# Kernel tuning notes

Hardware: AMD Instinct MI355X
Metric: run time of the kernel (lower is better)

## Reference

```python
import jax, jax.numpy as jnp
import numpy as np

B, S, H, NH = 2, 2048, 1024, 16
DK = H // NH

def setup_inputs() -> dict:
    key = jax.random.key(0)
    ks = jax.random.split(key, 12)
    scale = 0.02
    return {
        "Q": jax.random.normal(ks[0], (B, S, H), jnp.float32),
        "K": jax.random.normal(ks[1], (B, S, H), jnp.float32),
        "V": jax.random.normal(ks[2], (B, S, H), jnp.float32),
        "attn_mask": jax.random.randint(ks[3], (B, S, S), 0, 2).astype(bool),
        "Wq": jax.random.normal(ks[4], (H, H), jnp.float32) * scale,
        "bq": jnp.zeros((H,), jnp.float32),
        "Wk": jax.random.normal(ks[5], (H, H), jnp.float32) * scale,
        "bk": jnp.zeros((H,), jnp.float32),
        "Wv": jax.random.normal(ks[6], (H, H), jnp.float32) * scale,
        "bv": jnp.zeros((H,), jnp.float32),
        "Wo": jax.random.normal(ks[7], (H, H), jnp.float32) * scale,
        "bo": jnp.zeros((H,), jnp.float32),
    }

def reference(Q, K, V, attn_mask, Wq, bq, Wk, bk, Wv, bv, Wo, bo):
    b = Q.shape[0]
    # linear projections (torch nn.Linear: x @ W.T + b), split heads -> [b, nh, s, dk]
    def proj(x, W, bias):
        return (x @ W.T + bias).reshape(b, -1, NH, DK).transpose(0, 2, 1, 3)
    q = proj(Q, Wq, bq)
    k = proj(K, Wk, bk)
    v = proj(V, Wv, bv)
    scores = jnp.einsum("bhqd,bhkd->bhqk", q, k) / jnp.sqrt(jnp.float32(DK))
    scores = jnp.where(attn_mask[:, None, :, :], jnp.float32(-1e9), scores)
    attn = jax.nn.softmax(scores, axis=-1)  # dropout prob = 0.0 (identity)
    ctx = jnp.einsum("bhqk,bhkd->bhqd", attn, v)
    ctx = ctx.transpose(0, 2, 1, 3).reshape(b, -1, NH * DK)
    return ctx @ Wo.T + bo
```

## Files before the change

kernel.cpp:

```cpp
#include <hip/hip_runtime.h>

typedef short s16x8 __attribute__((ext_vector_type(8)));
typedef float f32x4 __attribute__((ext_vector_type(4)));
typedef unsigned short u16;
typedef unsigned int u32;
typedef unsigned long long u64;

#define DEVI __device__ __forceinline__

#if __has_builtin(__builtin_amdgcn_exp2f)
#define EXP2F(x) __builtin_amdgcn_exp2f(x)
#else
#define EXP2F(x) exp2f(x)
#endif

#define QSCALE 0.1803368801111204f

DEVI float bf2f(u16 u){ union { u32 i; float f; } v; v.i = ((u32)u) << 16; return v.f; }
DEVI u16 f2bf(float f){ union { float f; u32 i; } v; v.f = f; u32 u = v.i;
                        return (u16)((u + 0x7fffu + ((u >> 16) & 1u)) >> 16); }
DEVI u32 pack2r(float a, float b){
  union { float f; u32 i; } ua, ub; ua.f = a; ub.f = b;
  return ((ua.i + 0x8000u) >> 16) | ((ub.i + 0x8000u) & 0xffff0000u);
}
DEVI u64 pack4(float a, float b, float c, float d){
  return (u64)f2bf(a) | ((u64)f2bf(b) << 16) | ((u64)f2bf(c) << 32) | ((u64)f2bf(d) << 48);
}

DEVI f32x4 mfma_bf16(s16x8 a, s16x8 b, f32x4 c){
  return __builtin_amdgcn_mfma_f32_16x16x32_bf16(a, b, c, 0, 0, 0);
}

#define GLDS(gp, lp) __builtin_amdgcn_global_load_lds( \
    (const __attribute__((address_space(1))) void*)(gp), \
    (__attribute__((address_space(3))) void*)(lp), 16, 0, 0)

DEVI float4 cvt8f32(const float* p){
  float4 x = *(const float4*)p;
  float4 y = *(const float4*)(p + 4);
  union { u16 t[8]; float4 f4; } u;
  u.t[0] = f2bf(x.x); u.t[1] = f2bf(x.y); u.t[2] = f2bf(x.z); u.t[3] = f2bf(x.w);
  u.t[4] = f2bf(y.x); u.t[5] = f2bf(y.y); u.t[6] = f2bf(y.z); u.t[7] = f2bf(y.w);
  return u.f4;
}

DEVI bool detect_f32(const u16* probe){
  __shared__ int dsum[4];
  const int tid = threadIdx.x;
  int bad = 0;
#pragma unroll
  for (int i = 0; i < 16; ++i){
    u16 u = probe[tid * 16 + i];
    int e = (u >> 7) & 0xFF;
    bad += (e != 0 && (e < 100 || e > 150)) ? 1 : 0;
  }
#pragma unroll
  for (int o = 1; o < 64; o <<= 1) bad += __shfl_xor(bad, o);
  if ((tid & 63) == 0) dsum[tid >> 6] = bad;
  __syncthreads();
  bool r = (dsum[0] + dsum[1] + dsum[2] + dsum[3]) > 64;
  __syncthreads();
  return r;
}

struct PrepArgs { const void* src[7]; void* dst[7]; u32 coff[8]; };

__global__ __launch_bounds__(256) void prep(PrepArgs a, const u16* probe){
  const bool f32 = detect_f32(probe);
  if (!f32) return;
  const u32 total = a.coff[7];
  for (u32 c = blockIdx.x * 256 + threadIdx.x; c < total; c += gridDim.x * 256){
    int s = 0;
#pragma unroll
    for (int i = 1; i < 7; ++i) s += (c >= a.coff[i]) ? 1 : 0;
    u32 lc = c - a.coff[s];
    ((float4*)a.dst[s])[lc] = cvt8f32((const float*)a.src[s] + (size_t)lc * 8);
  }
}

__global__ __launch_bounds__(256) void maskpack(const int* __restrict__ mask,
                                                u64* __restrict__ bits){
  const int lane = threadIdx.x & 63, wid = threadIdx.x >> 6;
  const int row = blockIdx.x * 4 + wid;
  const int* mrow = mask + (size_t)row * 2048;
  for (int c = 0; c < 32; ++c){
    int v = mrow[c * 64 + lane];
    u64 w = __ballot(v == 0);
    if (lane == 0) bits[(size_t)row * 32 + c] = w;
  }
}

struct ProjP {
  const void* X[3];   const u16* Xc[3];
  const void* W[3];   const u16* Wc[3];
  const void* bias[3];
  u16* out[3];
  const u16* probe;
  int conv_ok;
};

__global__ __launch_bounds__(256) void proj_gemm(ProjP p){
  __shared__ u16 As[128 * 64];
  __shared__ u16 Bs[128 * 64];
  const int z = blockIdx.z;
  const bool in32 = detect_f32(p.probe);
  const bool f32st = in32 && !p.conv_ok;
  const u16* Ab = (in32 && p.conv_ok) ? p.Xc[z] : (const u16*)p.X[z];
  const u16* Wb = (in32 && p.conv_ok) ? p.Wc[z] : (const u16*)p.W[z];
  const float* Af = (const float*)p.X[z];
  const float* Wf = (const float*)p.W[z];
  const int tid = threadIdx.x;
  const int lane = tid & 63, wid = tid >> 6;
  const int quad = lane >> 4, l15 = lane & 15;
  const int m0 = blockIdx.y * 128, n0 = blockIdx.x * 128;
  const int wm = (wid >> 1) * 64, wn = (wid & 1) * 64;
  const int K = 1024;

  f32x4 acc[4][4];
  const f32x4 z4 = {0.f, 0.f, 0.f, 0.f};
  for (int i = 0; i < 4; ++i) for (int j = 0; j < 4; ++j) acc[i][j] = z4;

  for (int ko = 0; ko < 16; ++ko){
    const int kk = ko * 64;
    if (f32st){
#pragma unroll
      for (int i = 0; i < 4; ++i){
        int g = tid * 4 + i;
        int row = g >> 3, c = g & 7;
        *(float4*)(As + row * 64 + ((c ^ (row & 7)) * 8)) =
            cvt8f32(Af + (size_t)(m0 + row) * K + kk + c * 8);
        *(float4*)(Bs + row * 64 + ((c ^ (row & 7)) * 8)) =
            cvt8f32(Wf + (size_t)(n0 + row) * K + kk + c * 8);
      }
    } else {
#pragma unroll
      for (int i = 0; i < 4; ++i){
        int ci = (wid * 4 + i) * 64 + lane;
        int row = ci >> 3, gcc = (ci & 7) ^ (row & 7);
        GLDS(Ab + (size_t)(m0 + row) * K + kk + gcc * 8, As + (size_t)(wid * 4 + i) * 512);
        GLDS(Wb + (size_t)(n0 + row) * K + kk + gcc * 8, Bs + (size_t)(wid * 4 + i) * 512);
      }
    }
    __syncthreads();
#pragma unroll
    for (int ks = 0; ks < 2; ++ks){
      s16x8 af[4], bfr[4];
#pragma unroll
      for (int mt = 0; mt < 4; ++mt){
        int row = wm + mt * 16 + l15;
        af[mt] = *(const s16x8*)(As + row * 64 + (((ks * 4 + quad) ^ (row & 7)) * 8));
      }
#pragma unroll
      for (int nt = 0; nt < 4; ++nt){
        int row = wn + nt * 16 + l15;
        bfr[nt] = *(const s16x8*)(Bs + row * 64 + (((ks * 4 + quad) ^ (row & 7)) * 8));
      }
#pragma unroll
      for (int mt = 0; mt < 4; ++mt)
#pragma unroll
        for (int nt = 0; nt < 4; ++nt)
          acc[mt][nt] = mfma_bf16(af[mt], bfr[nt], acc[mt][nt]);
    }
    __syncthreads();
  }

  u16* outp = p.out[z];
#pragma unroll
  for (int nt = 0; nt < 4; ++nt){
    int col = n0 + wn + nt * 16 + l15;
    float bv = in32 ? ((const float*)p.bias[z])[col] : bf2f(((const u16*)p.bias[z])[col]);
#pragma unroll
    for (int mt = 0; mt < 4; ++mt){
      if (z == 2){
        int srow = m0 + wm + mt * 16 + quad * 4;
        int b = srow >> 11, s = srow & 2047, hh = col >> 6, d = col & 63;
        size_t idx = (((size_t)(b * 16 + hh)) * 64 + d) * 2048 + s;
        *(u64*)(outp + idx) = pack4(acc[mt][nt][0] + bv, acc[mt][nt][1] + bv,
                                    acc[mt][nt][2] + bv, acc[mt][nt][3] + bv);
      } else {
#pragma unroll
        for (int r = 0; r < 4; ++r){
          int row = m0 + wm + mt * 16 + quad * 4 + r;
          float v = acc[mt][nt][r] + bv;
          if (z == 0) v *= QSCALE;
          int b = row >> 11, s = row & 2047, hh = col >> 6, d = col & 63;
          outp[(((size_t)(b * 16 + hh)) * 2048 + s) * 64 + d] = f2bf(v);
        }
      }
    }
  }
}

__global__ __launch_bounds__(256) void gemm_out(const u16* __restrict__ A,
                                                const void* __restrict__ Wv,
                                                const u16* __restrict__ Wbf,
                                                const void* __restrict__ biasv,
                                                void* __restrict__ outv,
                                                const u16* __restrict__ probe,
                                                int conv_ok){
  __shared__ u16 As[64 * 64];
  __shared__ u16 Bs[128 * 64];
  const bool in32 = detect_f32(probe);
  const bool f32st = in32 && !conv_ok;
  const u16* Wb = (in32 && conv_ok) ? Wbf : (const u16*)Wv;
  const float* Wf = (const float*)Wv;
  const int tid = threadIdx.x;
  const int lane = tid & 63, wid = tid >> 6;
  const int quad = lane >> 4, l15 = lane & 15;
  const int m0 = blockIdx.y * 64, n0 = blockIdx.x * 128;
  const int wm = (wid >> 1) * 32, wn = (wid & 1) * 64;
  const int K = 1024;

  f32x4 acc[2][4];
  const f32x4 z4 = {0.f, 0.f, 0.f, 0.f};
  for (int i = 0; i < 2; ++i) for (int j = 0; j < 4; ++j) acc[i][j] = z4;

  for (int ko = 0; ko < 16; ++ko){
    const int kk = ko * 64;
#pragma unroll
    for (int i = 0; i < 2; ++i){
      int ci = (wid * 2 + i) * 64 + lane;
      int row = ci >> 3, gcc = (ci & 7) ^ (row & 7);
      GLDS(A + (size_t)(m0 + row) * K + kk + gcc * 8, As + (size_t)(wid * 2 + i) * 512);
    }
    if (f32st){
#pragma unroll
      for (int i = 0; i < 4; ++i){
        int g = tid * 4 + i;
        int row = g >> 3, c = g & 7;
        *(float4*)(Bs + row * 64 + ((c ^ (row & 7)) * 8)) =
            cvt8f32(Wf + (size_t)(n0 + row) * K + kk + c * 8);
      }
    } else {
#pragma unroll
      for (int i = 0; i < 4; ++i){
        int ci = (wid * 4 + i) * 64 + lane;
        int row = ci >> 3, gcc = (ci & 7) ^ (row & 7);
        GLDS(Wb + (size_t)(n0 + row) * K + kk + gcc * 8, Bs + (size_t)(wid * 4 + i) * 512);
      }
    }
    __syncthreads();
#pragma unroll
    for (int ks = 0; ks < 2; ++ks){
      s16x8 af[2], bfr[4];
#pragma unroll
      for (int mt = 0; mt < 2; ++mt){
        int row = wm + mt * 16 + l15;
        af[mt] = *(const s16x8*)(As + row * 64 + (((ks * 4 + quad) ^ (row & 7)) * 8));
      }
#pragma unroll
      for (int nt = 0; nt < 4; ++nt){
        int row = wn + nt * 16 + l15;
        bfr[nt] = *(const s16x8*)(Bs + row * 64 + (((ks * 4 + quad) ^ (row & 7)) * 8));
      }
#pragma unroll
      for (int mt = 0; mt < 2; ++mt)
#pragma unroll
        for (int nt = 0; nt < 4; ++nt)
          acc[mt][nt] = mfma_bf16(af[mt], bfr[nt], acc[mt][nt]);
    }
    __syncthreads();
  }

#pragma unroll
  for (int nt = 0; nt < 4; ++nt){
    int col = n0 + wn + nt * 16 + l15;
    float bv = in32 ? ((const float*)biasv)[col] : bf2f(((const u16*)biasv)[col]);
#pragma unroll
    for (int mt = 0; mt < 2; ++mt)
#pragma unroll
      for (int r = 0; r < 4; ++r){
        int row = m0 + wm + mt * 16 + quad * 4 + r;
        float v = acc[mt][nt][r] + bv;
        size_t idx = (size_t)row * 1024 + col;
        if (in32) ((float*)outv)[idx] = v;
        else      ((u16*)outv)[idx]   = f2bf(v);
      }
  }
}

__global__ __launch_bounds__(256) void attn2(const u16* __restrict__ qws,
                                             const u16* __restrict__ kws,
                                             const u16* __restrict__ vtws,
                                             const u64* __restrict__ mbits,
                                             const int* __restrict__ rawmask,
                                             int use_raw,
                                             u16* __restrict__ ctxws){
  __shared__ u16 Ks[64 * 64];
  __shared__ u16 Vt[64 * 64];
  __shared__ u16 Ps[4][16 * 64];
  const int tid = threadIdx.x;
  const int lane = tid & 63, wid = tid >> 6;
  const int quad = lane >> 4, l15 = lane & 15;
  const int h = blockIdx.x, qt = blockIdx.y, b = blockIdx.z;
  const int q0 = qt * 64;
  const size_t bh = (size_t)(b * 16 + h) * (2048 * 64);
  const int qrow = q0 + wid * 16 + l15;

  s16x8 qf[2];
#pragma unroll
  for (int ks = 0; ks < 2; ++ks)
    qf[ks] = *(const s16x8*)(qws + bh + (size_t)qrow * 64 + ks * 32 + quad * 8);

  const f32x4 z4 = {0.f, 0.f, 0.f, 0.f};
  f32x4 ctx[4];
  for (int dt = 0; dt < 4; ++dt) ctx[dt] = z4;
  float lr = 0.f;

  u16* pp = &Ps[wid][0];
  u32 pw[4];
#pragma unroll
  for (int ntk = 0; ntk < 4; ++ntk)
    pw[ntk] = l15 * 64 + (((u32)(ntk * 2 + (quad >> 1)) ^ (u32)(l15 & 7)) * 8) + (quad & 1) * 4;

  const u64* mrow = mbits + ((size_t)(b * 2048 + qrow)) * 32;

  for (int kt = 0; kt < 32; ++kt){
    const int k0 = kt * 64;
#pragma unroll
    for (int i = 0; i < 2; ++i){
      int ci = (wid * 2 + i) * 64 + lane;
      int row = ci >> 3, gcc = (ci & 7) ^ (row & 7);
      GLDS(kws + bh + (size_t)(k0 + row) * 64 + gcc * 8, Ks + (size_t)(wid * 2 + i) * 512);
      GLDS(vtws + bh + (size_t)row * 2048 + k0 + gcc * 8, Vt + (size_t)(wid * 2 + i) * 512);
    }
    __syncthreads();

    f32x4 s[4];
    for (int ntk = 0; ntk < 4; ++ntk) s[ntk] = z4;
#pragma unroll
    for (int ks = 0; ks < 2; ++ks)
#pragma unroll
      for (int ntk = 0; ntk < 4; ++ntk){
        int row = ntk * 16 + l15;
        s16x8 kf = *(const s16x8*)(Ks + row * 64 + (((ks * 4 + quad) ^ (row & 7)) * 8));
        s[ntk] = mfma_bf16(kf, qf[ks], s[ntk]);
      }

    float ls = 0.f;
    if (!use_raw){
      u64 w = mrow[kt] >> (quad * 4);
      u32 wlo = (u32)w, whi = (u32)(w >> 32);
#pragma unroll
      for (int ntk = 0; ntk < 4; ++ntk){
        u32 half = (ntk < 2) ? wlo : whi;
#pragma unroll
        for (int r = 0; r < 4; ++r){
          float pv = EXP2F(s[ntk][r]);
          u32 bit = (half >> ((ntk & 1) * 16 + r)) & 1u;
          pv *= (float)bit;
          s[ntk][r] = pv;
          ls += pv;
        }
      }
    } else {
#pragma unroll
      for (int ntk = 0; ntk < 4; ++ntk)
#pragma unroll
        for (int r = 0; r < 4; ++r){
          int key = k0 + ntk * 16 + quad * 4 + r;
          int mv = rawmask[((size_t)(b * 2048 + qrow)) * 2048 + key];
          float pv = EXP2F(s[ntk][r]);
          pv = mv ? 0.f : pv;
          s[ntk][r] = pv;
          ls += pv;
        }
    }
    lr += ls;

#pragma unroll
    for (int ntk = 0; ntk < 4; ++ntk){
      uint2 t;
      t.x = pack2r(s[ntk][0], s[ntk][1]);
      t.y = pack2r(s[ntk][2], s[ntk][3]);
      *(uint2*)(pp + pw[ntk]) = t;
    }
    s16x8 pf[2];
#pragma unroll
    for (int ks = 0; ks < 2; ++ks)
      pf[ks] = *(const s16x8*)(pp + l15 * 64 + (((ks * 4 + quad) ^ (l15 & 7)) * 8));

#pragma unroll
    for (int ks = 0; ks < 2; ++ks)
#pragma unroll
      for (int dt = 0; dt < 4; ++dt){
        int row = dt * 16 + l15;
        s16x8 vf = *(const s16x8*)(Vt + row * 64 + (((ks * 4 + quad) ^ (row & 7)) * 8));
        ctx[dt] = mfma_bf16(vf, pf[ks], ctx[dt]);
      }
    __syncthreads();
  }

  lr += __shfl_xor(lr, 16);
  lr += __shfl_xor(lr, 32);
  float inv = 1.0f / fmaxf(lr, 1e-30f);

#pragma unroll
  for (int dt = 0; dt < 4; ++dt){
    int d0 = dt * 16 + quad * 4;
    u64 w = pack4(ctx[dt][0] * inv, ctx[dt][1] * inv, ctx[dt][2] * inv, ctx[dt][3] * inv);
    *(u64*)(ctxws + ((size_t)(b * 2048 + qrow)) * 1024 + h * 64 + d0) = w;
  }
}

extern "C" void kernel_launch(void* const* d_in, const int* in_sizes, int n_in,
                              void* d_out, int out_size, void* d_ws, size_t ws_size,
                              hipStream_t stream){
  const void* Q    = d_in[0];
  const void* Kin  = d_in[1];
  const void* Vin  = d_in[2];
  const int* mask  = (const int*)d_in[3];
  const void* Wq = d_in[4];  const void* bq = d_in[5];
  const void* Wk = d_in[6];  const void* bk = d_in[7];
  const void* Wv = d_in[8];  const void* bv = d_in[9];
  const void* Wo = d_in[10]; const void* bo = d_in[11];

  char* ws = (char*)d_ws;
  const size_t MB = 1u << 20;
  const bool small_ws = ws_size < 33 * MB;
  const bool big_ws   = ws_size >= 66 * MB;
  u64* mbits = (u64*)ws;
  const size_t base = small_ws ? 0 : MB;
  u16* qws  = (u16*)(ws + base);
  u16* kws  = (u16*)(ws + base + 8 * MB);
  u16* vtws = (u16*)(ws + base + 16 * MB);
  u16* cws  = (u16*)(ws + base + 24 * MB);
  u16* Qc  = (u16*)(ws + 33 * MB);
  u16* Kc  = (u16*)(ws + 41 * MB);
  u16* Vc  = (u16*)(ws + 49 * MB);
  u16* Wqc = (u16*)(ws + 57 * MB);
  u16* Wkc = (u16*)(ws + 59 * MB);
  u16* Wvc = (u16*)(ws + 61 * MB);
  u16* Woc = (u16*)(ws + 63 * MB);
  const u16* probe = (const u16*)Q;

  if (big_ws){
    PrepArgs pa;
    pa.src[0] = Q;  pa.src[1] = Kin; pa.src[2] = Vin;
    pa.src[3] = Wq; pa.src[4] = Wk;  pa.src[5] = Wv; pa.src[6] = Wo;
    pa.dst[0] = Qc;  pa.dst[1] = Kc;  pa.dst[2] = Vc;
    pa.dst[3] = Wqc; pa.dst[4] = Wkc; pa.dst[5] = Wvc; pa.dst[6] = Woc;
    const u32 cq = 4194304 / 8, cw = 1048576 / 8;
    pa.coff[0] = 0;
    pa.coff[1] = cq;          pa.coff[2] = 2 * cq;      pa.coff[3] = 3 * cq;
    pa.coff[4] = 3 * cq + cw; pa.coff[5] = 3 * cq + 2 * cw;
    pa.coff[6] = 3 * cq + 3 * cw; pa.coff[7] = 3 * cq + 4 * cw;
    prep<<<dim3(2048), 256, 0, stream>>>(pa, probe);
  }

  if (!small_ws)
    maskpack<<<dim3(1024), 256, 0, stream>>>(mask, mbits);

  ProjP pp;
  pp.X[0] = Q;  pp.X[1] = Kin; pp.X[2] = Vin;
  pp.Xc[0] = Qc; pp.Xc[1] = Kc; pp.Xc[2] = Vc;
  pp.W[0] = Wq; pp.W[1] = Wk; pp.W[2] = Wv;
  pp.Wc[0] = Wqc; pp.Wc[1] = Wkc; pp.Wc[2] = Wvc;
  pp.bias[0] = bq; pp.bias[1] = bk; pp.bias[2] = bv;
  pp.out[0] = qws; pp.out[1] = kws; pp.out[2] = vtws;
  pp.probe = probe;
  pp.conv_ok = big_ws ? 1 : 0;
  proj_gemm<<<dim3(8, 32, 3), 256, 0, stream>>>(pp);

  attn2<<<dim3(16, 32, 2), 256, 0, stream>>>(qws, kws, vtws, mbits, mask,
                                             small_ws ? 1 : 0, cws);

  gemm_out<<<dim3(8, 64), 256, 0, stream>>>(cws, Wo, Woc, bo, d_out, probe,
                                            big_ws ? 1 : 0);
}
```

Before: 292.6 us.

## Split attention over key range, compute row sums via MFMA, mask via bitwise AND

Splits the key loop of the attention kernel into two halves across extra blocks (split-K), writing partial normalized contexts and row sums, then adds a combine kernel that merges them. The row sum of probabilities is now accumulated with an extra MFMA against a ones vector instead of scalar adds and shuffles. Mask application becomes a bitwise AND on packed bf16 pairs. These are meant to raise occupancy and parallelism (grid of 1024 blocks is doubled) and cut VALU work, at the cost of extra partial-result traffic, an extra launch, and a bf16 rounding of the partials before combining.

```diff
diff --git a/kernel.cpp b/kernel.cpp
--- a/kernel.cpp
+++ b/kernel.cpp
@@ -25,6 +25,9 @@
 }
 DEVI u64 pack4(float a, float b, float c, float d){
   return (u64)f2bf(a) | ((u64)f2bf(b) << 16) | ((u64)f2bf(c) << 32) | ((u64)f2bf(d) << 48);
+}
+DEVI u32 expand2(u32 t){
+  return ((t & 1u) * 0xFFFFu) + ((t & 2u) * 0x7FFF8000u);
 }
 
 DEVI f32x4 mfma_bf16(s16x8 a, s16x8 b, f32x4 c){
@@ -279,20 +282,24 @@
   }
 }
 
-__global__ __launch_bounds__(256) void attn2(const u16* __restrict__ qws,
-                                             const u16* __restrict__ kws,
-                                             const u16* __restrict__ vtws,
-                                             const u64* __restrict__ mbits,
-                                             const int* __restrict__ rawmask,
-                                             int use_raw,
-                                             u16* __restrict__ ctxws){
+__global__ __launch_bounds__(256, 6) void attn2(const u16* __restrict__ qws,
+                                                const u16* __restrict__ kws,
+                                                const u16* __restrict__ vtws,
+                                                const u64* __restrict__ mbits,
+                                                const int* __restrict__ rawmask,
+                                                int use_raw, int nsplit,
+                                                u16* __restrict__ outp,
+                                                float* __restrict__ lp){
   __shared__ u16 Ks[64 * 64];
   __shared__ u16 Vt[64 * 64];
   __shared__ u16 Ps[4][16 * 64];
   const int tid = threadIdx.x;
   const int lane = tid & 63, wid = tid >> 6;
   const int quad = lane >> 4, l15 = lane & 15;
-  const int h = blockIdx.x, qt = blockIdx.y, b = blockIdx.z;
+  const int h = blockIdx.x, qt = blockIdx.y;
+  const int b  = blockIdx.z / nsplit;
+  const int sp = blockIdx.z % nsplit;
+  const int ktn = 32 / nsplit, kt0 = sp * ktn;
   const int q0 = qt * 64;
   const size_t bh = (size_t)(b * 16 + h) * (2048 * 64);
   const int qrow = q0 + wid * 16 + l15;
@@ -302,10 +309,16 @@
   for (int ks = 0; ks < 2; ++ks)
     qf[ks] = *(const s16x8*)(qws + bh + (size_t)qrow * 64 + ks * 32 + quad * 8);
 
+  s16x8 af1;
+  {
+    short o = (l15 == 0) ? (short)0x3F80 : (short)0;
+    af1 = (s16x8){o, o, o, o, o, o, o, o};
+  }
+
   const f32x4 z4 = {0.f, 0.f, 0.f, 0.f};
   f32x4 ctx[4];
   for (int dt = 0; dt < 4; ++dt) ctx[dt] = z4;
-  float lr = 0.f;
+  f32x4 lacc = z4;
 
   u16* pp = &Ps[wid][0];
   u32 pw[4];
@@ -315,7 +328,7 @@
 
   const u64* mrow = mbits + ((size_t)(b * 2048 + qrow)) * 32;
 
-  for (int kt = 0; kt < 32; ++kt){
+  for (int kt = kt0; kt < kt0 + ktn; ++kt){
     const int k0 = kt * 64;
 #pragma unroll
     for (int i = 0; i < 2; ++i){
@@ -337,70 +350,97 @@
         s[ntk] = mfma_bf16(kf, qf[ks], s[ntk]);
       }
 
-    float ls = 0.f;
+    u32 m01[4], m23[4];
     if (!use_raw){
-      u64 w = mrow[kt] >> (quad * 4);
-      u32 wlo = (u32)w, whi = (u32)(w >> 32);
+      u64 wsh = mrow[kt] >> (quad * 4);
 #pragma unroll
       for (int ntk = 0; ntk < 4; ++ntk){
-        u32 half = (ntk < 2) ? wlo : whi;
-#pragma unroll
-        for (int r = 0; r < 4; ++r){
-          float pv = EXP2F(s[ntk][r]);
-          u32 bit = (half >> ((ntk & 1) * 16 + r)) & 1u;
-          pv *= (float)bit;
-          s[ntk][r] = pv;
-          ls += pv;
-        }
-      }
-    } else {
-#pragma unroll
-      for (int ntk = 0; ntk < 4; ++ntk)
-#pragma unroll
-        for (int r = 0; r < 4; ++r){
-          int key = k0 + ntk * 16 + quad * 4 + r;
-          int mv = rawmask[((size_t)(b * 2048 + qrow)) * 2048 + key];
-          float pv = EXP2F(s[ntk][r]);
-          pv = mv ? 0.f : pv;
-          s[ntk][r] = pv;
-          ls += pv;
-        }
-    }
-    lr += ls;
+        u32 t = (u32)(wsh >> (ntk * 16));
+        m01[ntk] = expand2(t);
+        m23[ntk] = expand2(t >> 2);
+      }
+    }
 
 #pragma unroll
     for (int ntk = 0; ntk < 4; ++ntk){
-      uint2 t;
-      t.x = pack2r(s[ntk][0], s[ntk][1]);
-      t.y = pack2r(s[ntk][2], s[ntk][3]);
-      *(uint2*)(pp + pw[ntk]) = t;
-    }
+      float p0 = EXP2F(s[ntk][0]), p1 = EXP2F(s[ntk][1]);
+      float p2 = EXP2F(s[ntk][2]), p3 = EXP2F(s[ntk][3]);
+      if (use_raw){
+        const int* mr = rawmask + ((size_t)(b * 2048 + qrow)) * 2048 + k0 + ntk * 16 + quad * 4;
+        p0 = mr[0] ? 0.f : p0;  p1 = mr[1] ? 0.f : p1;
+        p2 = mr[2] ? 0.f : p2;  p3 = mr[3] ? 0.f : p3;
+      }
+      u32 a01 = pack2r(p0, p1), a23 = pack2r(p2, p3);
+      if (!use_raw){ a01 &= m01[ntk]; a23 &= m23[ntk]; }
+      volatile u32* vp = (volatile u32*)(pp + pw[ntk]);
+      vp[0] = a01;
+      vp[1] = a23;
+    }
+    asm volatile("" ::: "memory");
+
     s16x8 pf[2];
 #pragma unroll
     for (int ks = 0; ks < 2; ++ks)
       pf[ks] = *(const s16x8*)(pp + l15 * 64 + (((ks * 4 + quad) ^ (l15 & 7)) * 8));
 
 #pragma unroll
-    for (int ks = 0; ks < 2; ++ks)
+    for (int ks = 0; ks < 2; ++ks){
 #pragma unroll
       for (int dt = 0; dt < 4; ++dt){
         int row = dt * 16 + l15;
         s16x8 vf = *(const s16x8*)(Vt + row * 64 + (((ks * 4 + quad) ^ (row & 7)) * 8));
         ctx[dt] = mfma_bf16(vf, pf[ks], ctx[dt]);
       }
+      lacc = mfma_bf16(af1, pf[ks], lacc);
+    }
     __syncthreads();
   }
 
-  lr += __shfl_xor(lr, 16);
-  lr += __shfl_xor(lr, 32);
-  float inv = 1.0f / fmaxf(lr, 1e-30f);
-
-#pragma unroll
-  for (int dt = 0; dt < 4; ++dt){
-    int d0 = dt * 16 + quad * 4;
-    u64 w = pack4(ctx[dt][0] * inv, ctx[dt][1] * inv, ctx[dt][2] * inv, ctx[dt][3] * inv);
-    *(u64*)(ctxws + ((size_t)(b * 2048 + qrow)) * 1024 + h * 64 + d0) = w;
-  }
+  float lv = __shfl(lacc[0], l15);
+  float inv = 1.0f / fmaxf(lv, 1e-30f);
+
+  if (nsplit == 1){
+#pragma unroll
+    for (int dt = 0; dt < 4; ++dt){
+      int d0 = dt * 16 + quad * 4;
+      u64 w = pack4(ctx[dt][0] * inv, ctx[dt][1] * inv, ctx[dt][2] * inv, ctx[dt][3] * inv);
+      *(u64*)(outp + ((size_t)(b * 2048 + qrow)) * 1024 + h * 64 + d0) = w;
+    }
+  } else {
+    u16* ob = outp + (size_t)sp * (4096u * 1024u);
+#pragma unroll
+    for (int dt = 0; dt < 4; ++dt){
+      int d0 = dt * 16 + quad * 4;
+      u64 w = pack4(ctx[dt][0] * inv, ctx[dt][1] * inv, ctx[dt][2] * inv, ctx[dt][3] * inv);
+      *(u64*)(ob + ((size_t)(b * 2048 + qrow)) * 1024 + h * 64 + d0) = w;
+    }
+    if (quad == 0)
+      lp[(size_t)sp * (4096u * 16u) + ((size_t)(b * 2048 + qrow)) * 16 + h] = lv;
+  }
+}
+
+__global__ __launch_bounds__(256) void combine(const u16* __restrict__ ctxp,
+                                               const float* __restrict__ lp,
+                                               u16* __restrict__ cws){
+  int gi = blockIdx.x * 256 + threadIdx.x;
+  int row = gi >> 7, cg = gi & 127;
+  int h = cg >> 3;
+  float l1 = lp[row * 16 + h];
+  float l2 = lp[4096 * 16 + row * 16 + h];
+  float inv = 1.0f / fmaxf(l1 + l2, 1e-30f);
+  float w1 = l1 * inv, w2 = l2 * inv;
+  size_t off = (size_t)row * 1024 + cg * 8;
+  uint4 a = *(const uint4*)(ctxp + off);
+  uint4 bq = *(const uint4*)(ctxp + (size_t)4096 * 1024 + off);
+  uint4 o;
+  u32* ap = (u32*)&a; u32* bp = (u32*)&bq; u32* op = (u32*)&o;
+#pragma unroll
+  for (int i = 0; i < 4; ++i){
+    float alo = bf2f((u16)(ap[i] & 0xffff)), ahi = bf2f((u16)(ap[i] >> 16));
+    float blo = bf2f((u16)(bp[i] & 0xffff)), bhi = bf2f((u16)(bp[i] >> 16));
+    op[i] = pack2r(alo * w1 + blo * w2, ahi * w1 + bhi * w2);
+  }
+  *(uint4*)(cws + off) = o;
 }
 
 extern "C" void kernel_launch(void* const* d_in, const int* in_sizes, int n_in,
@@ -432,6 +472,8 @@
   u16* Wkc = (u16*)(ws + 59 * MB);
   u16* Wvc = (u16*)(ws + 61 * MB);
   u16* Woc = (u16*)(ws + 63 * MB);
+  u16*   ctxp = (u16*)(ws + 33 * MB);
+  float* lpar = (float*)(ws + 49 * MB);
   const u16* probe = (const u16*)Q;
 
   if (big_ws){
@@ -462,8 +504,12 @@
   pp.conv_ok = big_ws ? 1 : 0;
   proj_gemm<<<dim3(8, 32, 3), 256, 0, stream>>>(pp);
 
-  attn2<<<dim3(16, 32, 2), 256, 0, stream>>>(qws, kws, vtws, mbits, mask,
-                                             small_ws ? 1 : 0, cws);
+  const int nsplit = big_ws ? 2 : 1;
+  attn2<<<dim3(16, 32, 2 * nsplit), 256, 0, stream>>>(
+      qws, kws, vtws, mbits, mask, small_ws ? 1 : 0, nsplit,
+      nsplit == 2 ? ctxp : cws, lpar);
+  if (nsplit == 2)
+    combine<<<dim3(2048), 256, 0, stream>>>(ctxp, lpar, cws);
 
   gemm_out<<<dim3(8, 64), 256, 0, stream>>>(cws, Wo, Woc, bo, d_out, probe,
                                             big_ws ? 1 : 0);
```

Measured after the change: 452.8 us. 54.7% more time.
